# Optimization experiments

Hardware: AMD Instinct MI355X
Metric: run time of the kernel (lower is better)

The kernel has to match this reference:

```python
import jax, jax.numpy as jnp
import numpy as np
from jax import lax

EPS = 1e-12
CLS_K = 100   # cls-token prefilter size (hardcoded in patch_reconstruction)
ALPHA = 0.6   # weighting of cls vs patch-EMD distance (hardcoded in source)


def _l2norm(x, axis):
    # torch.nn.functional.normalize: x / max(||x||_2, eps)
    n = jnp.sqrt(jnp.sum(x * x, axis=axis, keepdims=True))
    return x / jnp.maximum(n, EPS)


def setup_inputs() -> dict:
    key = jax.random.key(0)
    k1, k2, k3, k4 = jax.random.split(key, 4)
    B, N, C, G = 16, 128, 768, 2000
    return {
        "query_cls": jax.random.normal(k1, (B, C), dtype=jnp.float32),
        "query_patch": jax.random.normal(k2, (B, N, C), dtype=jnp.float32),
        "gallery_memory_cls": jax.random.normal(k3, (G, 1, C), dtype=jnp.float32),
        "gallery_memory_patch": jax.random.normal(k4, (G, N, C), dtype=jnp.float32),
        "top_k": 10,
    }


def reference(query_cls, query_patch, gallery_memory_cls, gallery_memory_patch, top_k):
    B, N, C = query_patch.shape
    g_cls = gallery_memory_cls[:, 0, :]          # [G, C] (torch.squeeze)
    g_cls_n = _l2norm(g_cls, axis=1)             # normalize(gallery_feat, dim=1)

    def per_sample(qc, qp):
        # --- stage 1: cls-token cosine prefilter (find_k_neighbors, metric='cls_token')
        qc_n = _l2norm(qc, axis=0)               # [C]
        dist_cls_all = g_cls_n @ qc_n            # [G] cosine sim
        _, cls_idx = lax.top_k(dist_cls_all, CLS_K)   # top-100 by cls sim

        # --- stage 2: combined cls + patch-EMD score over the 100 candidates
        sq = _l2norm(qp.T, axis=0)               # [C, N] per-patch unit norm
        gp = gallery_memory_patch[cls_idx]       # [K, N, C] gather
        gp_t = _l2norm(jnp.transpose(gp, (0, 2, 1)), axis=1)  # [K, C, N]
        # pairwise patch cosine sims: [K, Nq, Ng]
        sim = jnp.einsum('cn,kcm->knm', sq, gp_t)
        # bidirectional Chamfer similarity as the patch-EMD score
        dist_emd = 0.5 * (jnp.mean(jnp.max(sim, axis=2), axis=1)
                          + jnp.mean(jnp.max(sim, axis=1), axis=1))  # [K]
        dist_cls = dist_cls_all[cls_idx]         # [K]
        dist = ALPHA * dist_cls + (1.0 - ALPHA) * dist_emd
        _, emd_idx = lax.top_k(dist, top_k)      # top_k of 100 candidates
        nb = cls_idx[emd_idx]                    # [top_k] gallery indices

        # --- reconstruction: gather neighbor patches + mean neighbor cls
        patch = gallery_memory_patch[nb]         # [top_k, N, C]
        cls_m = jnp.mean(g_cls[nb], axis=0)      # [C]
        return patch.reshape(top_k * N, C), cls_m

    rec_patch, rec_cls = jax.vmap(per_sample)(query_cls, query_patch)
    return rec_patch, rec_cls[:, None, :]        # [B, top_k*N, C], [B, 1, C]
```

## Files before the change

### kernel.cpp

```cpp
#include <hip/hip_runtime.h>
#include <float.h>
#include <math.h>

#define B_ 16
#define N_ 128
#define C_ 768
#define G_ 2000
#define CK_ 100
#define ALPHA_ 0.6f
#define EPS_ 1e-12f

typedef __attribute__((ext_vector_type(8))) short bf16x8;
typedef __attribute__((ext_vector_type(16))) float f32x16;

__device__ inline float wave_sum_lane0(float s) {
  #pragma unroll
  for (int off = 32; off > 0; off >>= 1) s += __shfl_down(s, off);
  return s;
}
__device__ inline float wave_sum_all(float s) {
  #pragma unroll
  for (int off = 1; off < 64; off <<= 1) s += __shfl_xor(s, off);
  return s;
}

__device__ inline unsigned short bf16_rtn(float x) {
  unsigned u = __float_as_uint(x);
  u += 0x7fffu + ((u >> 16) & 1u);
  return (unsigned short)(u >> 16);
}
__device__ inline void split2(float x, unsigned short& h, unsigned short& l) {
  h = bf16_rtn(x);
  float r = x - __uint_as_float(((unsigned)h) << 16);
  l = bf16_rtn(r);
}
__device__ inline void tsplit8(const float4& v0, const float4& v1,
                               uint4& h, uint4& l, float& sq) {
  float f[8] = {v0.x, v0.y, v0.z, v0.w, v1.x, v1.y, v1.z, v1.w};
  unsigned hu[4], lu[4];
  #pragma unroll
  for (int p = 0; p < 4; ++p) {
    float x0 = f[2 * p], x1 = f[2 * p + 1];
    sq = fmaf(x0, x0, sq);
    sq = fmaf(x1, x1, sq);
    unsigned u0 = __float_as_uint(x0), u1 = __float_as_uint(x1);
    float r0 = x0 - __uint_as_float(u0 & 0xFFFF0000u);
    float r1 = x1 - __uint_as_float(u1 & 0xFFFF0000u);
    unsigned v0b = __float_as_uint(r0), v1b = __float_as_uint(r1);
    hu[p] = (u0 >> 16) | (u1 & 0xFFFF0000u);
    lu[p] = (v0b >> 16) | (v1b & 0xFFFF0000u);
  }
  h = make_uint4(hu[0], hu[1], hu[2], hu[3]);
  l = make_uint4(lu[0], lu[1], lu[2], lu[3]);
}

#define NCLSBLK_ (B_ * G_ / 4)
__global__ void prep_kernel(const float* __restrict__ gcls, const float* __restrict__ qcls,
                            const float* __restrict__ qp,
                            float* __restrict__ dall,
                            unsigned short* __restrict__ qhi, unsigned short* __restrict__ qlo) {
  int t = threadIdx.x;
  int lane = t & 63;
  if ((int)blockIdx.x < NCLSBLK_) {
    int id = ((int)blockIdx.x * 256 + t) >> 6;
    int b = id / G_, g = id - b * G_;
    const float4* gv = (const float4*)(gcls + (size_t)g * C_);
    const float4* qv = (const float4*)(qcls + (size_t)b * C_);
    float sgq = 0.f, sgg = 0.f, sqq = 0.f;
    #pragma unroll
    for (int i = 0; i < 3; ++i) {
      float4 x = gv[lane + 64 * i], y = qv[lane + 64 * i];
      sgq += x.x * y.x + x.y * y.y + x.z * y.z + x.w * y.w;
      sgg += x.x * x.x + x.y * x.y + x.z * x.z + x.w * x.w;
      sqq += y.x * y.x + y.y * y.y + y.z * y.z + y.w * y.w;
    }
    sgq = wave_sum_lane0(sgq);
    sgg = wave_sum_lane0(sgg);
    sqq = wave_sum_lane0(sqq);
    if (lane == 0) {
      float gi = 1.0f / fmaxf(sqrtf(sgg), EPS_);
      float qi = 1.0f / fmaxf(sqrtf(sqq), EPS_);
      dall[id] = sgq * gi * qi;
    }
  } else {
    int wid = (((int)blockIdx.x - NCLSBLK_) * 256 + t) >> 6;
    const float4* v = (const float4*)(qp + (size_t)wid * C_);
    float4 x0 = v[lane], x1 = v[lane + 64], x2 = v[lane + 128];
    float s = x0.x * x0.x + x0.y * x0.y + x0.z * x0.z + x0.w * x0.w
            + x1.x * x1.x + x1.y * x1.y + x1.z * x1.z + x1.w * x1.w
            + x2.x * x2.x + x2.y * x2.y + x2.z * x2.z + x2.w * x2.w;
    s = wave_sum_all(s);
    float inv = 1.0f / fmaxf(sqrtf(s), EPS_);
    float4 xs[3] = {x0, x1, x2};
    #pragma unroll
    for (int i = 0; i < 3; ++i) {
      float4 x = xs[i];
      x.x *= inv; x.y *= inv; x.z *= inv; x.w *= inv;
      ushort4 h, l;
      split2(x.x, h.x, l.x); split2(x.y, h.y, l.y);
      split2(x.z, h.z, l.z); split2(x.w, h.w, l.w);
      size_t off = (size_t)wid * C_ + (size_t)(lane + 64 * i) * 4;
      *(ushort4*)(qhi + off) = h;
      *(ushort4*)(qlo + off) = l;
    }
  }
}

__global__ void top100_kernel(const float* __restrict__ dall, int* __restrict__ cls_idx,
                              float* __restrict__ dsel) {
  __shared__ unsigned long long s[2048];
  int b = blockIdx.x, t = threadIdx.x;
  for (int i = t; i < 2048; i += 256) {
    unsigned long long y = 0xFFFFFFFFFFFFFFFFull;
    if (i < G_) {
      unsigned u = __float_as_uint(dall[b * G_ + i]);
      unsigned key = (u & 0x80000000u) ? ~u : (u | 0x80000000u);
      y = ~(((unsigned long long)key << 32) | (unsigned long long)(0xFFFFFFFFu - (unsigned)i));
    }
    s[i] = y;
  }
  __syncthreads();
  for (int k = 2; k <= 2048; k <<= 1) {
    for (int j = k >> 1; j > 0; j >>= 1) {
      for (int i = t; i < 2048; i += 256) {
        int l = i ^ j;
        if (l > i) {
          unsigned long long a = s[i], c = s[l];
          bool up = ((i & k) == 0);
          if ((a > c) == up) { s[i] = c; s[l] = a; }
        }
      }
      __syncthreads();
    }
  }
  for (int it = t; it < CK_; it += 256) {
    unsigned long long x = ~s[it];
    int idx = (int)(0xFFFFFFFFu - (unsigned)(x & 0xFFFFFFFFull));
    unsigned key = (unsigned)(x >> 32);
    unsigned u = (key & 0x80000000u) ? (key & 0x7FFFFFFFu) : ~key;
    cls_idx[b * CK_ + it] = idx;
    dsel[b * CK_ + it] = __uint_as_float(u);
  }
}

__global__ __launch_bounds__(256, 2) void emd_kernel(
    const unsigned short* __restrict__ qhi, const unsigned short* __restrict__ qlo,
    const float* __restrict__ gpat,
    const int* __restrict__ cls_idx, const float* __restrict__ dsel,
    float* __restrict__ dist) {
  __shared__ __align__(16) unsigned short sAhi[2][4096], sAlo[2][4096];
  __shared__ __align__(16) unsigned short sBhi[2][4096], sBlo[2][4096];
  float* red_row = (float*)&sAhi[0][0];
  float* red_col = (float*)&sAhi[0][512];
  float* bssf    = (float*)&sAhi[0][1024];
  float* binvf   = (float*)&sAhi[0][1536];

  int r = blockIdx.x;
  int xc = r & 7;
  int q = r >> 3;
  int b = 2 * xc + (q >= CK_ ? 1 : 0);
  int k = (q >= CK_) ? (q - CK_) : q;
  int blk = b * CK_ + k;
  int g = cls_idx[blk];

  const float* Bptr = gpat + (size_t)g * (N_ * C_);

  int t = threadIdx.x;
  int lane = t & 63, wv = t >> 6;
  int wr = wv >> 1, wc = wv & 1;
  int l31 = lane & 31, lhi = lane >> 5;

  int m_st = t >> 1, half = t & 1;
  const unsigned short* ahB = qhi + (size_t)(b * N_ + m_st) * C_ + half * 16;
  const unsigned short* alB = qlo + (size_t)(b * N_ + m_st) * C_ + half * 16;
  const float* bB = Bptr + (size_t)m_st * C_ + half * 16;
  int sw_st = (m_st >> 1) & 3;
  int e0 = m_st * 32 + (((2 * half + 0) ^ sw_st) << 3);
  int e1 = m_st * 32 + (((2 * half + 1) ^ sw_st) << 3);

  f32x16 acc00, acc01, acc10, acc11;
  #pragma unroll
  for (int e = 0; e < 16; ++e) { acc00[e] = 0.f; acc01[e] = 0.f; acc10[e] = 0.f; acc11[e] = 0.f; }

  int rA0 = 64 * wr + l31, rA1 = rA0 + 32;
  int rB0 = 64 * wc + l31, rB1 = rB0 + 32;
  int swF = (l31 >> 1) & 3;

  const int NT = C_ / 32;

  float bsq = 0.f;

  uint4 cah0, cah1, cal0, cal1;
  float4 bx0, bx1, bx2, bx3, by0, by1, by2, by3;

#define LOAD_A(T) { int oA = (T) * 32;                                        \
    cah0 = *(const uint4*)(ahB + oA);  cah1 = *(const uint4*)(ahB + oA + 8);  \
    cal0 = *(const uint4*)(alB + oA);  cal1 = *(const uint4*)(alB + oA + 8); }
#define LOAD_BX(T) { int oB = (T) * 32;                                       \
    bx0 = *(const float4*)(bB + oB);      bx1 = *(const float4*)(bB + oB + 4);\
    bx2 = *(const float4*)(bB + oB + 8);  bx3 = *(const float4*)(bB + oB + 12); }
#define LOAD_BY(T) { int oB = (T) * 32;                                       \
    by0 = *(const float4*)(bB + oB);      by1 = *(const float4*)(bB + oB + 4);\
    by2 = *(const float4*)(bB + oB + 8);  by3 = *(const float4*)(bB + oB + 12); }

#define STAGE(P, Bq0, Bq1, Bq2, Bq3) {                                        \
    uint4 h, l;                                                               \
    tsplit8(Bq0, Bq1, h, l, bsq);                                             \
    *(uint4*)&sBhi[P][e0] = h;  *(uint4*)&sBlo[P][e0] = l;                    \
    tsplit8(Bq2, Bq3, h, l, bsq);                                             \
    *(uint4*)&sBhi[P][e1] = h;  *(uint4*)&sBlo[P][e1] = l;                    \
    *(uint4*)&sAhi[P][e0] = cah0;  *(uint4*)&sAhi[P][e1] = cah1;              \
    *(uint4*)&sAlo[P][e0] = cal0;  *(uint4*)&sAlo[P][e1] = cal1;              \
  }

#define MFMA_PHASE(P)                                                         \
  _Pragma("unroll")                                                           \
  for (int ks = 0; ks < 2; ++ks) {                                            \
    int so = (((ks * 2 + lhi) ^ swF) << 3);                                   \
    bf16x8 ah0 = *(const bf16x8*)&sAhi[P][rA0 * 32 + so];                     \
    bf16x8 al0 = *(const bf16x8*)&sAlo[P][rA0 * 32 + so];                     \
    bf16x8 ah1 = *(const bf16x8*)&sAhi[P][rA1 * 32 + so];                     \
    bf16x8 al1 = *(const bf16x8*)&sAlo[P][rA1 * 32 + so];                     \
    bf16x8 bh0 = *(const bf16x8*)&sBhi[P][rB0 * 32 + so];                     \
    bf16x8 bl0 = *(const bf16x8*)&sBlo[P][rB0 * 32 + so];                     \
    bf16x8 bh1 = *(const bf16x8*)&sBhi[P][rB1 * 32 + so];                     \
    bf16x8 bl1 = *(const bf16x8*)&sBlo[P][rB1 * 32 + so];                     \
    acc00 = __builtin_amdgcn_mfma_f32_32x32x16_bf16(ah0, bh0, acc00, 0, 0, 0);\
    acc00 = __builtin_amdgcn_mfma_f32_32x32x16_bf16(ah0, bl0, acc00, 0, 0, 0);\
    acc00 = __builtin_amdgcn_mfma_f32_32x32x16_bf16(al0, bh0, acc00, 0, 0, 0);\
    acc01 = __builtin_amdgcn_mfma_f32_32x32x16_bf16(ah0, bh1, acc01, 0, 0, 0);\
    acc01 = __builtin_amdgcn_mfma_f32_32x32x16_bf16(ah0, bl1, acc01, 0, 0, 0);\
    acc01 = __builtin_amdgcn_mfma_f32_32x32x16_bf16(al0, bh1, acc01, 0, 0, 0);\
    acc10 = __builtin_amdgcn_mfma_f32_32x32x16_bf16(ah1, bh0, acc10, 0, 0, 0);\
    acc10 = __builtin_amdgcn_mfma_f32_32x32x16_bf16(ah1, bl0, acc10, 0, 0, 0);\
    acc10 = __builtin_amdgcn_mfma_f32_32x32x16_bf16(al1, bh0, acc10, 0, 0, 0);\
    acc11 = __builtin_amdgcn_mfma_f32_32x32x16_bf16(ah1, bh1, acc11, 0, 0, 0);\
    acc11 = __builtin_amdgcn_mfma_f32_32x32x16_bf16(ah1, bl1, acc11, 0, 0, 0);\
    acc11 = __builtin_amdgcn_mfma_f32_32x32x16_bf16(al1, bh1, acc11, 0, 0, 0);\
  }

  LOAD_A(0);
  LOAD_BX(0);
  LOAD_BY(1);
  STAGE(0, bx0, bx1, bx2, bx3);
  LOAD_A(1);
  LOAD_BX(2);
  __syncthreads();

  for (int kt = 0; kt < NT; kt += 2) {
    if (kt + 1 < NT) STAGE(1, by0, by1, by2, by3);
    if (kt + 2 < NT) LOAD_A(kt + 2);
    if (kt + 3 < NT) LOAD_BY(kt + 3);
    MFMA_PHASE(0);
    __syncthreads();
    if (kt + 1 < NT) {
      if (kt + 2 < NT) STAGE(0, bx0, bx1, bx2, bx3);
      if (kt + 3 < NT) LOAD_A(kt + 3);
      if (kt + 4 < NT) LOAD_BX(kt + 4);
      MFMA_PHASE(1);
    }
    __syncthreads();
  }
#undef LOAD_A
#undef LOAD_BX
#undef LOAD_BY
#undef STAGE
#undef MFMA_PHASE

  bssf[t] = bsq;
  __syncthreads();
  if (t < 128) {
    float s = bssf[2 * t] + bssf[2 * t + 1];
    binvf[t] = 1.0f / fmaxf(sqrtf(s), EPS_);
  }
  __syncthreads();
  float bi0 = binvf[64 * wc + l31];
  float bi1 = binvf[64 * wc + 32 + l31];

  {
    float rm[16];
    #pragma unroll
    for (int e = 0; e < 16; ++e) rm[e] = fmaxf(acc00[e] * bi0, acc01[e] * bi1);
    #pragma unroll
    for (int msk = 1; msk <= 16; msk <<= 1)
      #pragma unroll
      for (int e = 0; e < 16; ++e) rm[e] = fmaxf(rm[e], __shfl_xor(rm[e], msk));
    if (l31 == 0) {
      #pragma unroll
      for (int e = 0; e < 16; ++e)
        red_row[(64 * wr + (e & 3) + 8 * (e >> 2) + 4 * lhi) * 2 + wc] = rm[e];
    }
  }
  {
    float rm[16];
    #pragma unroll
    for (int e = 0; e < 16; ++e) rm[e] = fmaxf(acc10[e] * bi0, acc11[e] * bi1);
    #pragma unroll
    for (int msk = 1; msk <= 16; msk <<= 1)
      #pragma unroll
      for (int e = 0; e < 16; ++e) rm[e] = fmaxf(rm[e], __shfl_xor(rm[e], msk));
    if (l31 == 0) {
      #pragma unroll
      for (int e = 0; e < 16; ++e)
        red_row[(64 * wr + 32 + (e & 3) + 8 * (e >> 2) + 4 * lhi) * 2 + wc] = rm[e];
    }
  }
  {
    float cm0 = -FLT_MAX, cm1 = -FLT_MAX;
    #pragma unroll
    for (int e = 0; e < 16; ++e) {
      cm0 = fmaxf(cm0, fmaxf(acc00[e], acc10[e]));
      cm1 = fmaxf(cm1, fmaxf(acc01[e], acc11[e]));
    }
    cm0 = fmaxf(cm0, __shfl_xor(cm0, 32)) * bi0;
    cm1 = fmaxf(cm1, __shfl_xor(cm1, 32)) * bi1;
    if (lane < 32) {
      red_col[(64 * wc + lane) * 2 + wr] = cm0;
      red_col[(64 * wc + 32 + lane) * 2 + wr] = cm1;
    }
  }
  __syncthreads();
  if (t < 128)
    bssf[t] = fmaxf(red_row[2 * t], red_row[2 * t + 1]) +
              fmaxf(red_col[2 * t], red_col[2 * t + 1]);
  __syncthreads();
  if (t < 64) {
    float v = bssf[t] + bssf[t + 64];
    #pragma unroll
    for (int off = 32; off > 0; off >>= 1) v += __shfl_down(v, off);
    if (t == 0) {
      float emd = 0.5f * v * (1.0f / 128.0f);
      dist[blk] = ALPHA_ * dsel[blk] + (1.0f - ALPHA_) * emd;
    }
  }
}

__global__ void sel10_kernel(const float* __restrict__ dist, const int* __restrict__ cls_idx,
                             const float* __restrict__ gcls, float* __restrict__ out_cls,
                             int* __restrict__ nb, int TK) {
  int b = blockIdx.x, t = threadIdx.x;
  __shared__ float v[128];
  __shared__ int snb[64];
  if (t < 128) v[t] = (t < CK_) ? dist[b * CK_ + t] : -FLT_MAX;
  __syncthreads();
  for (int j = 0; j < TK; ++j) {
    if (t < 64) {
      float v0 = v[t], v1 = v[t + 64];
      float bv; int bi;
      if (v0 >= v1) { bv = v0; bi = t; } else { bv = v1; bi = t + 64; }
      #pragma unroll
      for (int off = 1; off < 64; off <<= 1) {
        float ov = __shfl_xor(bv, off);
        int   oi = __shfl_xor(bi, off);
        if (ov > bv || (ov == bv && oi < bi)) { bv = ov; bi = oi; }
      }
      if (t == 0) {
        int gg = cls_idx[b * CK_ + bi];
        snb[j] = gg;
        nb[b * TK + j] = gg;
        v[bi] = -FLT_MAX;
      }
    }
    __syncthreads();
  }
  float invk = 1.0f / (float)TK;
  for (int c = t; c < C_; c += 256) {
    float s = 0.f;
    for (int j = 0; j < TK; ++j) s += gcls[(size_t)snb[j] * C_ + c];
    out_cls[(size_t)b * C_ + c] = s * invk;
  }
}

__global__ void gather_kernel(const float* __restrict__ gpat, const int* __restrict__ nb,
                              float* __restrict__ out, int TK) {
  int i = blockIdx.x * blockDim.x + threadIdx.x;
  int per_vec = N_ * C_ / 4;
  int per_b = TK * per_vec;
  int total = B_ * per_b;
  if (i >= total) return;
  int b = i / per_b;
  int r = i - b * per_b;
  int j = r / per_vec;
  int off = r - j * per_vec;
  int g = nb[b * TK + j];
  ((float4*)out)[i] = ((const float4*)gpat)[(size_t)g * per_vec + off];
}

extern "C" void kernel_launch(void* const* d_in, const int* in_sizes, int n_in,
                              void* d_out, int out_size, void* d_ws, size_t ws_size,
                              hipStream_t stream) {
  (void)in_sizes; (void)n_in; (void)ws_size;
  const float* qcls = (const float*)d_in[0];
  const float* qpat = (const float*)d_in[1];
  const float* gcls = (const float*)d_in[2];
  const float* gpat = (const float*)d_in[3];
  int TK = (out_size / B_ - C_) / (N_ * C_);

  unsigned short* qhi = (unsigned short*)d_ws;
  unsigned short* qlo = qhi + (size_t)B_ * N_ * C_;
  float* dall  = (float*)(qlo + (size_t)B_ * N_ * C_);
  float* dsel  = dall + B_ * G_;
  float* dist  = dsel + B_ * CK_;
  int* cls_idx = (int*)(dist + B_ * CK_);
  int* nb      = cls_idx + B_ * CK_;

  hipLaunchKernelGGL(prep_kernel, dim3(NCLSBLK_ + B_ * N_ / 4), dim3(256), 0, stream,
                     gcls, qcls, qpat, dall, qhi, qlo);
  hipLaunchKernelGGL(top100_kernel, dim3(B_), dim3(256), 0, stream, dall, cls_idx, dsel);
  hipLaunchKernelGGL(emd_kernel, dim3(B_ * CK_), dim3(256), 0, stream,
                     qhi, qlo, gpat, cls_idx, dsel, dist);
  float* out_cls = (float*)d_out + (size_t)B_ * TK * N_ * C_;
  hipLaunchKernelGGL(sel10_kernel, dim3(B_), dim3(256), 0, stream,
                     dist, cls_idx, gcls, out_cls, nb, TK);
  int total4 = B_ * TK * (N_ * C_ / 4);
  hipLaunchKernelGGL(gather_kernel, dim3((total4 + 255) / 256), dim3(256), 0, stream,
                     gpat, nb, (float*)d_out, TK);
}
```

Before: 315.0 us.

## Pre-pack query split operands in MFMA fragment layout and load directly from global

The prep kernel now writes the normalized query hi/lo bf16 split in a layout that matches the per-lane MFMA A-fragment order. The EMD kernel reads A fragments straight from global/L2 memory instead of staging them through shared memory. This removes the A-tile LDS stores and reads and halves the shared memory footprint, which may allow more occupancy. In exchange, the global loads for A sit inside the MFMA phase without software prefetch, so their latency may be exposed.

```diff
diff --git a/kernel.cpp b/kernel.cpp
--- a/kernel.cpp
+++ b/kernel.cpp
@@ -9,6 +9,8 @@
 #define CK_ 100
 #define ALPHA_ 0.6f
 #define EPS_ 1e-12f
+
+#define ASTRIDE_B_ (N_ * C_ * 2)
 
 typedef __attribute__((ext_vector_type(8))) short bf16x8;
 typedef __attribute__((ext_vector_type(16))) float f32x16;
@@ -58,7 +60,7 @@
 __global__ void prep_kernel(const float* __restrict__ gcls, const float* __restrict__ qcls,
                             const float* __restrict__ qp,
                             float* __restrict__ dall,
-                            unsigned short* __restrict__ qhi, unsigned short* __restrict__ qlo) {
+                            unsigned short* __restrict__ qsp) {
   int t = threadIdx.x;
   int lane = t & 63;
   if ((int)blockIdx.x < NCLSBLK_) {
@@ -84,24 +86,49 @@
     }
   } else {
     int wid = (((int)blockIdx.x - NCLSBLK_) * 256 + t) >> 6;
-    const float4* v = (const float4*)(qp + (size_t)wid * C_);
-    float4 x0 = v[lane], x1 = v[lane + 64], x2 = v[lane + 128];
+    int b = wid >> 7, rr = wid & 127;
+    int j = rr >> 5, l31p = rr & 31;
+    const float* row = qp + (size_t)wid * C_;
+    float4 x0 = *(const float4*)(row + lane * 8);
+    float4 x1 = *(const float4*)(row + lane * 8 + 4);
+    float4 x2 = make_float4(0.f, 0.f, 0.f, 0.f), x3 = x2;
+    if (lane < 32) {
+      x2 = *(const float4*)(row + 512 + lane * 8);
+      x3 = *(const float4*)(row + 512 + lane * 8 + 4);
+    }
     float s = x0.x * x0.x + x0.y * x0.y + x0.z * x0.z + x0.w * x0.w
             + x1.x * x1.x + x1.y * x1.y + x1.z * x1.z + x1.w * x1.w
-            + x2.x * x2.x + x2.y * x2.y + x2.z * x2.z + x2.w * x2.w;
+            + x2.x * x2.x + x2.y * x2.y + x2.z * x2.z + x2.w * x2.w
+            + x3.x * x3.x + x3.y * x3.y + x3.z * x3.z + x3.w * x3.w;
     s = wave_sum_all(s);
     float inv = 1.0f / fmaxf(sqrtf(s), EPS_);
-    float4 xs[3] = {x0, x1, x2};
-    #pragma unroll
-    for (int i = 0; i < 3; ++i) {
-      float4 x = xs[i];
-      x.x *= inv; x.y *= inv; x.z *= inv; x.w *= inv;
-      ushort4 h, l;
-      split2(x.x, h.x, l.x); split2(x.y, h.y, l.y);
-      split2(x.z, h.z, l.z); split2(x.w, h.w, l.w);
-      size_t off = (size_t)wid * C_ + (size_t)(lane + 64 * i) * 4;
-      *(ushort4*)(qhi + off) = h;
-      *(ushort4*)(qlo + off) = l;
+    size_t bj = (size_t)b * ASTRIDE_B_ + (size_t)j * 2048;
+    #pragma unroll
+    for (int half = 0; half < 2; ++half) {
+      if (half == 1 && lane >= 32) break;
+      int c = half == 0 ? lane : 64 + lane;
+      float4 v0 = half == 0 ? x0 : x2;
+      float4 v1 = half == 0 ? x1 : x3;
+      v0.x *= inv; v0.y *= inv; v0.z *= inv; v0.w *= inv;
+      v1.x *= inv; v1.y *= inv; v1.z *= inv; v1.w *= inv;
+      float f[8] = {v0.x, v0.y, v0.z, v0.w, v1.x, v1.y, v1.z, v1.w};
+      unsigned short hh[8], ll[8];
+      #pragma unroll
+      for (int i = 0; i < 8; ++i) split2(f[i], hh[i], ll[i]);
+      uint4 hq, lq;
+      hq.x = (unsigned)hh[0] | ((unsigned)hh[1] << 16);
+      hq.y = (unsigned)hh[2] | ((unsigned)hh[3] << 16);
+      hq.z = (unsigned)hh[4] | ((unsigned)hh[5] << 16);
+      hq.w = (unsigned)hh[6] | ((unsigned)hh[7] << 16);
+      lq.x = (unsigned)ll[0] | ((unsigned)ll[1] << 16);
+      lq.y = (unsigned)ll[2] | ((unsigned)ll[3] << 16);
+      lq.z = (unsigned)ll[4] | ((unsigned)ll[5] << 16);
+      lq.w = (unsigned)ll[6] | ((unsigned)ll[7] << 16);
+      int kt = c >> 2, ks = (c >> 1) & 1, lh = c & 1;
+      int lanef = lh * 32 + l31p;
+      size_t off = bj + (size_t)kt * 8192 + (size_t)ks * 1024 + (size_t)lanef * 8;
+      *(uint4*)(qsp + off) = hq;
+      *(uint4*)(qsp + off + 512) = lq;
     }
   }
 }
@@ -144,16 +171,15 @@
 }
 
 __global__ __launch_bounds__(256, 2) void emd_kernel(
-    const unsigned short* __restrict__ qhi, const unsigned short* __restrict__ qlo,
+    const unsigned short* __restrict__ qsp,
     const float* __restrict__ gpat,
     const int* __restrict__ cls_idx, const float* __restrict__ dsel,
     float* __restrict__ dist) {
-  __shared__ __align__(16) unsigned short sAhi[2][4096], sAlo[2][4096];
   __shared__ __align__(16) unsigned short sBhi[2][4096], sBlo[2][4096];
-  float* red_row = (float*)&sAhi[0][0];
-  float* red_col = (float*)&sAhi[0][512];
-  float* bssf    = (float*)&sAhi[0][1024];
-  float* binvf   = (float*)&sAhi[0][1536];
+  float* red_row = (float*)&sBhi[0][0];
+  float* red_col = (float*)&sBhi[0][512];
+  float* bssf    = (float*)&sBhi[0][1024];
+  float* binvf   = (float*)&sBhi[0][1536];
 
   int r = blockIdx.x;
   int xc = r & 7;
@@ -171,8 +197,6 @@
   int l31 = lane & 31, lhi = lane >> 5;
 
   int m_st = t >> 1, half = t & 1;
-  const unsigned short* ahB = qhi + (size_t)(b * N_ + m_st) * C_ + half * 16;
-  const unsigned short* alB = qlo + (size_t)(b * N_ + m_st) * C_ + half * 16;
   const float* bB = Bptr + (size_t)m_st * C_ + half * 16;
   int sw_st = (m_st >> 1) & 3;
   int e0 = m_st * 32 + (((2 * half + 0) ^ sw_st) << 3);
@@ -182,20 +206,17 @@
   #pragma unroll
   for (int e = 0; e < 16; ++e) { acc00[e] = 0.f; acc01[e] = 0.f; acc10[e] = 0.f; acc11[e] = 0.f; }
 
-  int rA0 = 64 * wr + l31, rA1 = rA0 + 32;
+  const unsigned short* aB = qsp + (size_t)b * ASTRIDE_B_ + (size_t)(2 * wr) * 2048
+                           + (size_t)lane * 8;
+
   int rB0 = 64 * wc + l31, rB1 = rB0 + 32;
   int swF = (l31 >> 1) & 3;
 
   const int NT = C_ / 32;
-
   float bsq = 0.f;
 
-  uint4 cah0, cah1, cal0, cal1;
   float4 bx0, bx1, bx2, bx3, by0, by1, by2, by3;
 
-#define LOAD_A(T) { int oA = (T) * 32;                                        \
-    cah0 = *(const uint4*)(ahB + oA);  cah1 = *(const uint4*)(ahB + oA + 8);  \
-    cal0 = *(const uint4*)(alB + oA);  cal1 = *(const uint4*)(alB + oA + 8); }
 #define LOAD_BX(T) { int oB = (T) * 32;                                       \
     bx0 = *(const float4*)(bB + oB);      bx1 = *(const float4*)(bB + oB + 4);\
     bx2 = *(const float4*)(bB + oB + 8);  bx3 = *(const float4*)(bB + oB + 12); }
@@ -209,59 +230,76 @@
     *(uint4*)&sBhi[P][e0] = h;  *(uint4*)&sBlo[P][e0] = l;                    \
     tsplit8(Bq2, Bq3, h, l, bsq);                                             \
     *(uint4*)&sBhi[P][e1] = h;  *(uint4*)&sBlo[P][e1] = l;                    \
-    *(uint4*)&sAhi[P][e0] = cah0;  *(uint4*)&sAhi[P][e1] = cah1;              \
-    *(uint4*)&sAlo[P][e0] = cal0;  *(uint4*)&sAlo[P][e1] = cal1;              \
-  }
-
-#define MFMA_PHASE(P)                                                         \
-  _Pragma("unroll")                                                           \
-  for (int ks = 0; ks < 2; ++ks) {                                            \
-    int so = (((ks * 2 + lhi) ^ swF) << 3);                                   \
-    bf16x8 ah0 = *(const bf16x8*)&sAhi[P][rA0 * 32 + so];                     \
-    bf16x8 al0 = *(const bf16x8*)&sAlo[P][rA0 * 32 + so];                     \
-    bf16x8 ah1 = *(const bf16x8*)&sAhi[P][rA1 * 32 + so];                     \
-    bf16x8 al1 = *(const bf16x8*)&sAlo[P][rA1 * 32 + so];                     \
-    bf16x8 bh0 = *(const bf16x8*)&sBhi[P][rB0 * 32 + so];                     \
-    bf16x8 bl0 = *(const bf16x8*)&sBlo[P][rB0 * 32 + so];                     \
-    bf16x8 bh1 = *(const bf16x8*)&sBhi[P][rB1 * 32 + so];                     \
-    bf16x8 bl1 = *(const bf16x8*)&sBlo[P][rB1 * 32 + so];                     \
-    acc00 = __builtin_amdgcn_mfma_f32_32x32x16_bf16(ah0, bh0, acc00, 0, 0, 0);\
-    acc00 = __builtin_amdgcn_mfma_f32_32x32x16_bf16(ah0, bl0, acc00, 0, 0, 0);\
-    acc00 = __builtin_amdgcn_mfma_f32_32x32x16_bf16(al0, bh0, acc00, 0, 0, 0);\
-    acc01 = __builtin_amdgcn_mfma_f32_32x32x16_bf16(ah0, bh1, acc01, 0, 0, 0);\
-    acc01 = __builtin_amdgcn_mfma_f32_32x32x16_bf16(ah0, bl1, acc01, 0, 0, 0);\
-    acc01 = __builtin_amdgcn_mfma_f32_32x32x16_bf16(al0, bh1, acc01, 0, 0, 0);\
-    acc10 = __builtin_amdgcn_mfma_f32_32x32x16_bf16(ah1, bh0, acc10, 0, 0, 0);\
-    acc10 = __builtin_amdgcn_mfma_f32_32x32x16_bf16(ah1, bl0, acc10, 0, 0, 0);\
-    acc10 = __builtin_amdgcn_mfma_f32_32x32x16_bf16(al1, bh0, acc10, 0, 0, 0);\
-    acc11 = __builtin_amdgcn_mfma_f32_32x32x16_bf16(ah1, bh1, acc11, 0, 0, 0);\
-    acc11 = __builtin_amdgcn_mfma_f32_32x32x16_bf16(ah1, bl1, acc11, 0, 0, 0);\
-    acc11 = __builtin_amdgcn_mfma_f32_32x32x16_bf16(al1, bh1, acc11, 0, 0, 0);\
-  }
-
-  LOAD_A(0);
+  }
+
+#define MFMA_PHASE(P, KT) {                                                   \
+    const unsigned short* ap = aB + (KT) * 8192;                              \
+    bf16x8 a00 = *(const bf16x8*)(ap);                           \
+    bf16x8 a01 = *(const bf16x8*)(ap + 512);                     \
+    bf16x8 a02 = *(const bf16x8*)(ap + 2048);                    \
+    bf16x8 a03 = *(const bf16x8*)(ap + 2560);                    \
+    bf16x8 a10 = *(const bf16x8*)(ap + 1024);                    \
+    bf16x8 a11 = *(const bf16x8*)(ap + 1536);                    \
+    bf16x8 a12 = *(const bf16x8*)(ap + 3072);                    \
+    bf16x8 a13 = *(const bf16x8*)(ap + 3584);                    \
+    {                                                                         \
+      int so = (((0 * 2 + lhi) ^ swF) << 3);                                  \
+      bf16x8 bh0 = *(const bf16x8*)&sBhi[P][rB0 * 32 + so];                   \
+      bf16x8 bl0 = *(const bf16x8*)&sBlo[P][rB0 * 32 + so];                   \
+      bf16x8 bh1 = *(const bf16x8*)&sBhi[P][rB1 * 32 + so];                   \
+      bf16x8 bl1 = *(const bf16x8*)&sBlo[P][rB1 * 32 + so];                   \
+      acc00 = __builtin_amdgcn_mfma_f32_32x32x16_bf16(a00, bh0, acc00, 0, 0, 0);\
+      acc00 = __builtin_amdgcn_mfma_f32_32x32x16_bf16(a00, bl0, acc00, 0, 0, 0);\
+      acc00 = __builtin_amdgcn_mfma_f32_32x32x16_bf16(a01, bh0, acc00, 0, 0, 0);\
+      acc01 = __builtin_amdgcn_mfma_f32_32x32x16_bf16(a00, bh1, acc01, 0, 0, 0);\
+      acc01 = __builtin_amdgcn_mfma_f32_32x32x16_bf16(a00, bl1, acc01, 0, 0, 0);\
+      acc01 = __builtin_amdgcn_mfma_f32_32x32x16_bf16(a01, bh1, acc01, 0, 0, 0);\
+      acc10 = __builtin_amdgcn_mfma_f32_32x32x16_bf16(a02, bh0, acc10, 0, 0, 0);\
+      acc10 = __builtin_amdgcn_mfma_f32_32x32x16_bf16(a02, bl0, acc10, 0, 0, 0);\
+      acc10 = __builtin_amdgcn_mfma_f32_32x32x16_bf16(a03, bh0, acc10, 0, 0, 0);\
+      acc11 = __builtin_amdgcn_mfma_f32_32x32x16_bf16(a02, bh1, acc11, 0, 0, 0);\
+      acc11 = __builtin_amdgcn_mfma_f32_32x32x16_bf16(a02, bl1, acc11, 0, 0, 0);\
+      acc11 = __builtin_amdgcn_mfma_f32_32x32x16_bf16(a03, bh1, acc11, 0, 0, 0);\
+    }                                                                         \
+    {                                                                         \
+      int so = (((1 * 2 + lhi) ^ swF) << 3);                                  \
+      bf16x8 bh0 = *(const bf16x8*)&sBhi[P][rB0 * 32 + so];                   \
+      bf16x8 bl0 = *(const bf16x8*)&sBlo[P][rB0 * 32 + so];                   \
+      bf16x8 bh1 = *(const bf16x8*)&sBhi[P][rB1 * 32 + so];                   \
+      bf16x8 bl1 = *(const bf16x8*)&sBlo[P][rB1 * 32 + so];                   \
+      acc00 = __builtin_amdgcn_mfma_f32_32x32x16_bf16(a10, bh0, acc00, 0, 0, 0);\
+      acc00 = __builtin_amdgcn_mfma_f32_32x32x16_bf16(a10, bl0, acc00, 0, 0, 0);\
+      acc00 = __builtin_amdgcn_mfma_f32_32x32x16_bf16(a11, bh0, acc00, 0, 0, 0);\
+      acc01 = __builtin_amdgcn_mfma_f32_32x32x16_bf16(a10, bh1, acc01, 0, 0, 0);\
+      acc01 = __builtin_amdgcn_mfma_f32_32x32x16_bf16(a10, bl1, acc01, 0, 0, 0);\
+      acc01 = __builtin_amdgcn_mfma_f32_32x32x16_bf16(a11, bh1, acc01, 0, 0, 0);\
+      acc10 = __builtin_amdgcn_mfma_f32_32x32x16_bf16(a12, bh0, acc10, 0, 0, 0);\
+      acc10 = __builtin_amdgcn_mfma_f32_32x32x16_bf16(a12, bl0, acc10, 0, 0, 0);\
+      acc10 = __builtin_amdgcn_mfma_f32_32x32x16_bf16(a13, bh0, acc10, 0, 0, 0);\
+      acc11 = __builtin_amdgcn_mfma_f32_32x32x16_bf16(a12, bh1, acc11, 0, 0, 0);\
+      acc11 = __builtin_amdgcn_mfma_f32_32x32x16_bf16(a12, bl1, acc11, 0, 0, 0);\
+      acc11 = __builtin_amdgcn_mfma_f32_32x32x16_bf16(a13, bh1, acc11, 0, 0, 0);\
+    }                                                                         \
+  }
+
   LOAD_BX(0);
   LOAD_BY(1);
   STAGE(0, bx0, bx1, bx2, bx3);
-  LOAD_A(1);
   LOAD_BX(2);
   __syncthreads();
 
   for (int kt = 0; kt < NT; kt += 2) {
     if (kt + 1 < NT) STAGE(1, by0, by1, by2, by3);
-    if (kt + 2 < NT) LOAD_A(kt + 2);
     if (kt + 3 < NT) LOAD_BY(kt + 3);
-    MFMA_PHASE(0);
+    MFMA_PHASE(0, kt);
     __syncthreads();
     if (kt + 1 < NT) {
       if (kt + 2 < NT) STAGE(0, bx0, bx1, bx2, bx3);
-      if (kt + 3 < NT) LOAD_A(kt + 3);
       if (kt + 4 < NT) LOAD_BX(kt + 4);
-      MFMA_PHASE(1);
+      MFMA_PHASE(1, kt + 1);
     }
     __syncthreads();
   }
-#undef LOAD_A
 #undef LOAD_BX
 #undef LOAD_BY
 #undef STAGE
@@ -396,19 +434,18 @@
   const float* gpat = (const float*)d_in[3];
   int TK = (out_size / B_ - C_) / (N_ * C_);
 
-  unsigned short* qhi = (unsigned short*)d_ws;
-  unsigned short* qlo = qhi + (size_t)B_ * N_ * C_;
-  float* dall  = (float*)(qlo + (size_t)B_ * N_ * C_);
+  unsigned short* qsp = (unsigned short*)d_ws;
+  float* dall  = (float*)(qsp + (size_t)B_ * ASTRIDE_B_);
   float* dsel  = dall + B_ * G_;
   float* dist  = dsel + B_ * CK_;
   int* cls_idx = (int*)(dist + B_ * CK_);
   int* nb      = cls_idx + B_ * CK_;
 
   hipLaunchKernelGGL(prep_kernel, dim3(NCLSBLK_ + B_ * N_ / 4), dim3(256), 0, stream,
-                     gcls, qcls, qpat, dall, qhi, qlo);
+                     gcls, qcls, qpat, dall, qsp);
   hipLaunchKernelGGL(top100_kernel, dim3(B_), dim3(256), 0, stream, dall, cls_idx, dsel);
   hipLaunchKernelGGL(emd_kernel, dim3(B_ * CK_), dim3(256), 0, stream,
-                     qhi, qlo, gpat, cls_idx, dsel, dist);
+                     qsp, gpat, cls_idx, dsel, dist);
   float* out_cls = (float*)d_out + (size_t)B_ * TK * N_ * C_;
   hipLaunchKernelGGL(sel10_kernel, dim3(B_), dim3(256), 0, stream,
                      dist, cls_idx, gcls, out_cls, nb, TK);
```

Result: slower. 326.1 us (+3.5%).
